# Kernel tuning notes

Measured on AMD Instinct MI355X. Metric: run time of the kernel, lower is better.

Reference implementation:

```python
import jax, jax.numpy as jnp
import numpy as np

E, I, H, T = 8, 2816, 1024, 8192

def setup_inputs() -> dict:
    key = jax.random.key(0)
    ks = jax.random.split(key, 5)
    scale_w = 1.0 / np.sqrt(H)
    return {
        "hidden_states": jax.random.normal(ks[0], (T, H), jnp.float32),
        "router_logits": jax.random.normal(ks[1], (T, E), jnp.float32),
        "W1": jax.random.normal(ks[2], (E, I, H), jnp.float32) * scale_w,
        "W3": jax.random.normal(ks[3], (E, I, H), jnp.float32) * scale_w,
        "W2": jax.random.normal(ks[4], (E, H, I), jnp.float32) * (1.0 / np.sqrt(I)),
        "top_k": 2,
    }

def reference(hidden_states, router_logits, W1, W3, W2, top_k):
    # softmax router in fp32, topk, renormalize (renormalize=True, use_grouped_topk=False)
    probs = jax.nn.softmax(router_logits.astype(jnp.float32), axis=-1)  # [T,E]
    vals, idx = jax.lax.top_k(probs, top_k)                             # [T,K]
    vals = vals / jnp.sum(vals, axis=-1, keepdims=True)
    vals = vals.astype(hidden_states.dtype)
    n_tok, n_exp = probs.shape
    # dense per-token expert weight matrix [T,E]; zero for unrouted experts,
    # mathematically identical to the gather/scatter-add in the ipex op
    w = jnp.zeros((n_tok, n_exp), hidden_states.dtype).at[
        jnp.arange(n_tok)[:, None], idx].add(vals)

    def expert_step(acc, args):
        We1, We3, We2, we = args  # [I,H], [I,H], [H,I], [T]
        h = jax.nn.silu(hidden_states @ We1.T) * (hidden_states @ We3.T)  # [T,I]
        return acc + we[:, None] * (h @ We2.T), None

    out, _ = jax.lax.scan(expert_step, jnp.zeros_like(hidden_states),
                          (W1, W3, W2, w.T))
    return out
```

## Files before the change

### kernel.cpp

```cpp
#include <hip/hip_runtime.h>
#include <stdint.h>

#define NE 8
#define NI 2816
#define NH 1024
#define NT 8192
#define NPAIR (NT * 2)

typedef __bf16 bf16x8 __attribute__((ext_vector_type(8)));
typedef float f32x4 __attribute__((ext_vector_type(4)));

__device__ __forceinline__ uint16_t f2bf(float f) {
    union { float f; uint32_t u; } v;
    v.f = f;
    return (uint16_t)((v.u + 0x7FFFu + ((v.u >> 16) & 1u)) >> 16);
}

__device__ __forceinline__ float bflo(uint32_t u) {
    union { uint32_t x; float f; } v; v.x = u << 16; return v.f;
}
__device__ __forceinline__ float bfhi(uint32_t u) {
    union { uint32_t x; float f; } v; v.x = u & 0xffff0000u; return v.f;
}

__device__ __forceinline__ void gld16(const void* g, void* l) {
    __builtin_amdgcn_global_load_lds(
        (__attribute__((address_space(1))) void*)(uintptr_t)g,
        (__attribute__((address_space(3))) void*)(uint32_t)(uintptr_t)l,
        16, 0, 0);
}

__global__ __launch_bounds__(256) void k_cvt3(const float* __restrict__ W1,
                                              const float* __restrict__ W3,
                                              const float* __restrict__ W2,
                                              uint16_t* __restrict__ W1b,
                                              uint16_t* __restrict__ W3b,
                                              uint16_t* __restrict__ W2b) {
    int i = blockIdx.x * 256 + threadIdx.x;
    const float* s = blockIdx.y == 0 ? W1 : (blockIdx.y == 1 ? W3 : W2);
    uint16_t* d = blockIdx.y == 0 ? W1b : (blockIdx.y == 1 ? W3b : W2b);
    float4 a = ((const float4*)s)[(size_t)i * 2];
    float4 b = ((const float4*)s)[(size_t)i * 2 + 1];
    uint4 o;
    o.x = (uint32_t)f2bf(a.x) | ((uint32_t)f2bf(a.y) << 16);
    o.y = (uint32_t)f2bf(a.z) | ((uint32_t)f2bf(a.w) << 16);
    o.z = (uint32_t)f2bf(b.x) | ((uint32_t)f2bf(b.y) << 16);
    o.w = (uint32_t)f2bf(b.z) | ((uint32_t)f2bf(b.w) << 16);
    ((uint4*)d)[i] = o;
}

__global__ __launch_bounds__(256) void k_router(const float* __restrict__ logits,
                                                int* __restrict__ tok_e,
                                                float2* __restrict__ tok_w,
                                                int* __restrict__ counts) {
    int t = blockIdx.x * 256 + threadIdx.x;
    if (t >= NT) return;
    float4 a = ((const float4*)logits)[(size_t)t * 2];
    float4 b = ((const float4*)logits)[(size_t)t * 2 + 1];
    float l[8] = {a.x, a.y, a.z, a.w, b.x, b.y, b.z, b.w};
    int i0 = 0; float l0 = l[0];
#pragma unroll
    for (int e = 1; e < 8; e++) if (l[e] > l0) { l0 = l[e]; i0 = e; }
    int i1 = -1; float l1 = -3.4e38f;
#pragma unroll
    for (int e = 0; e < 8; e++) if (e != i0 && l[e] > l1) { l1 = l[e]; i1 = e; }
    float w0 = 1.f / (1.f + __expf(l1 - l0));
    float w1 = 1.f - w0;
    tok_e[t] = i0 | (i1 << 8);
    tok_w[t] = make_float2(w0, w1);
    atomicAdd(&counts[i0], 1);
    atomicAdd(&counts[i1], 1);
}

__global__ void k_scan(const int* __restrict__ counts, int* __restrict__ offsets,
                       int* __restrict__ cursor) {
    if (threadIdx.x == 0) {
        int o = 0;
        for (int e = 0; e < NE; e++) { offsets[e] = o; cursor[e] = o; o += counts[e]; }
    }
}

__global__ __launch_bounds__(128) void k_gather(const float* __restrict__ x,
                                                const int* __restrict__ tok_e,
                                                const float2* __restrict__ tok_w,
                                                int* __restrict__ cursor,
                                                uint16_t* __restrict__ Xg,
                                                int2* __restrict__ tok_slots,
                                                float* __restrict__ slot_w) {
    int t = blockIdx.x;
    __shared__ int ss[2];
    if (threadIdx.x == 0) {
        int ee = tok_e[t];
        float2 w = tok_w[t];
        int s0 = atomicAdd(&cursor[ee & 0xff], 1);
        int s1 = atomicAdd(&cursor[(ee >> 8) & 0xff], 1);
        ss[0] = s0; ss[1] = s1;
        tok_slots[t] = make_int2(s0, s1);
        slot_w[s0] = w.x;
        slot_w[s1] = w.y;
    }
    __syncthreads();
    int s0 = ss[0], s1 = ss[1];
    int i = threadIdx.x;
    const float4* xr = (const float4*)(x + (size_t)t * NH);
    float4 a = xr[i * 2];
    float4 b = xr[i * 2 + 1];
    uint4 o;
    o.x = (uint32_t)f2bf(a.x) | ((uint32_t)f2bf(a.y) << 16);
    o.y = (uint32_t)f2bf(a.z) | ((uint32_t)f2bf(a.w) << 16);
    o.z = (uint32_t)f2bf(b.x) | ((uint32_t)f2bf(b.y) << 16);
    o.w = (uint32_t)f2bf(b.z) | ((uint32_t)f2bf(b.w) << 16);
    ((uint4*)(Xg + (size_t)s0 * NH))[i] = o;
    ((uint4*)(Xg + (size_t)s1 * NH))[i] = o;
}

__global__ __launch_bounds__(256, 2) void k_gemm1(const uint16_t* __restrict__ Xg,
                                                  const uint16_t* __restrict__ W1b,
                                                  const uint16_t* __restrict__ W3b,
                                                  uint16_t* __restrict__ Hbuf,
                                                  const int* __restrict__ counts,
                                                  const int* __restrict__ offsets) {
    int e = blockIdx.z;
    int n_e = counts[e];
    int mtile = blockIdx.y;
    if (mtile * 128 >= n_e) return;
    int ntile = blockIdx.x;
    int off = offsets[e];

    __shared__ __align__(16) uint16_t As[128 * 32];
    __shared__ __align__(16) uint16_t B1s[128 * 32];
    __shared__ __align__(16) uint16_t B3s[128 * 32];

    int tid = threadIdx.x;
    int r = tid >> 2, c = tid & 3;
    int wv = tid >> 6, lane = tid & 63;
    int wr = wv >> 1, wc = wv & 1;
    int m_in = lane & 15, q = lane >> 4;

    int rowA0 = off + mtile * 128 + r;
    int rowA1 = min(rowA0 + 64, NPAIR - 1);
    rowA0 = min(rowA0, NPAIR - 1);
    const uint16_t* a0 = Xg + (size_t)rowA0 * NH + c * 8;
    const uint16_t* a1 = Xg + (size_t)rowA1 * NH + c * 8;
    const uint16_t* b1r = W1b + ((size_t)e * NI + ntile * 128 + r) * NH + c * 8;
    const uint16_t* b3r = W3b + ((size_t)e * NI + ntile * 128 + r) * NH + c * 8;

    uint16_t* lA0 = &As[tid * 8];   uint16_t* lA1 = &As[2048 + tid * 8];
    uint16_t* lB10 = &B1s[tid * 8]; uint16_t* lB11 = &B1s[2048 + tid * 8];
    uint16_t* lB30 = &B3s[tid * 8]; uint16_t* lB31 = &B3s[2048 + tid * 8];

    const uint16_t* pa = &As[(wr * 64 + m_in) * 32 + q * 8];
    const uint16_t* pb1 = &B1s[(wc * 64 + m_in) * 32 + q * 8];
    const uint16_t* pb3 = &B3s[(wc * 64 + m_in) * 32 + q * 8];

    f32x4 acc1[4][4] = {};
    f32x4 acc3[4][4] = {};

    for (int k0 = 0; k0 < NH; k0 += 32) {
        gld16(a0 + k0, lA0);
        gld16(a1 + k0, lA1);
        gld16(b1r + k0, lB10);
        gld16(b1r + (size_t)64 * NH + k0, lB11);
        gld16(b3r + k0, lB30);
        gld16(b3r + (size_t)64 * NH + k0, lB31);
        __syncthreads();

        bf16x8 af[4], b1f[4], b3f[4];
#pragma unroll
        for (int it = 0; it < 4; it++) af[it] = *(const bf16x8*)(pa + it * 512);
#pragma unroll
        for (int jt = 0; jt < 4; jt++) {
            b1f[jt] = *(const bf16x8*)(pb1 + jt * 512);
            b3f[jt] = *(const bf16x8*)(pb3 + jt * 512);
        }
#pragma unroll
        for (int it = 0; it < 4; it++)
#pragma unroll
            for (int jt = 0; jt < 4; jt++) {
                acc1[it][jt] = __builtin_amdgcn_mfma_f32_16x16x32_bf16(af[it], b1f[jt], acc1[it][jt], 0, 0, 0);
                acc3[it][jt] = __builtin_amdgcn_mfma_f32_16x16x32_bf16(af[it], b3f[jt], acc3[it][jt], 0, 0, 0);
            }
        __syncthreads();
    }

    int sBase = off + mtile * 128;
#pragma unroll
    for (int it = 0; it < 4; it++) {
#pragma unroll
        for (int reg = 0; reg < 4; reg++) {
            int lm = wr * 64 + it * 16 + q * 4 + reg;
            if (mtile * 128 + lm < n_e) {
                uint16_t* orow = Hbuf + (size_t)(sBase + lm) * NI + ntile * 128 + wc * 64 + m_in;
#pragma unroll
                for (int jt = 0; jt < 4; jt++) {
                    float c1 = acc1[it][jt][reg];
                    float c3 = acc3[it][jt][reg];
                    float hv = (c1 / (1.f + __expf(-c1))) * c3;
                    orow[jt * 16] = f2bf(hv);
                }
            }
        }
    }
}

__global__ __launch_bounds__(256, 2) void k_gemm2(const uint16_t* __restrict__ Hbuf,
                                                  const uint16_t* __restrict__ W2b,
                                                  uint16_t* __restrict__ Ybuf,
                                                  const int* __restrict__ counts,
                                                  const int* __restrict__ offsets) {
    int e = blockIdx.z;
    int n_e = counts[e];
    int mtile = blockIdx.y;
    if (mtile * 128 >= n_e) return;
    int ntile = blockIdx.x;
    int off = offsets[e];

    __shared__ __align__(16) uint16_t As[128 * 32];
    __shared__ __align__(16) uint16_t Bs[128 * 32];

    int tid = threadIdx.x;
    int r = tid >> 2, c = tid & 3;
    int wv = tid >> 6, lane = tid & 63;
    int wr = wv >> 1, wc = wv & 1;
    int m_in = lane & 15, q = lane >> 4;

    int rowA0 = off + mtile * 128 + r;
    int rowA1 = min(rowA0 + 64, NPAIR - 1);
    rowA0 = min(rowA0, NPAIR - 1);
    const uint16_t* a0 = Hbuf + (size_t)rowA0 * NI + c * 8;
    const uint16_t* a1 = Hbuf + (size_t)rowA1 * NI + c * 8;
    const uint16_t* br = W2b + ((size_t)e * NH + ntile * 128 + r) * NI + c * 8;

    uint16_t* lA0 = &As[tid * 8]; uint16_t* lA1 = &As[2048 + tid * 8];
    uint16_t* lB0 = &Bs[tid * 8]; uint16_t* lB1 = &Bs[2048 + tid * 8];

    const uint16_t* pa = &As[(wr * 64 + m_in) * 32 + q * 8];
    const uint16_t* pb = &Bs[(wc * 64 + m_in) * 32 + q * 8];

    f32x4 acc[4][4] = {};

    for (int k0 = 0; k0 < NI; k0 += 32) {
        gld16(a0 + k0, lA0);
        gld16(a1 + k0, lA1);
        gld16(br + k0, lB0);
        gld16(br + (size_t)64 * NI + k0, lB1);
        __syncthreads();

        bf16x8 af[4], bf[4];
#pragma unroll
        for (int it = 0; it < 4; it++) af[it] = *(const bf16x8*)(pa + it * 512);
#pragma unroll
        for (int jt = 0; jt < 4; jt++) bf[jt] = *(const bf16x8*)(pb + jt * 512);
#pragma unroll
        for (int it = 0; it < 4; it++)
#pragma unroll
            for (int jt = 0; jt < 4; jt++)
                acc[it][jt] = __builtin_amdgcn_mfma_f32_16x16x32_bf16(af[it], bf[jt], acc[it][jt], 0, 0, 0);
        __syncthreads();
    }

    int sBase = off + mtile * 128;
#pragma unroll
    for (int it = 0; it < 4; it++) {
#pragma unroll
        for (int reg = 0; reg < 4; reg++) {
            int lm = wr * 64 + it * 16 + q * 4 + reg;
            if (mtile * 128 + lm < n_e) {
                uint16_t* orow = Ybuf + (size_t)(sBase + lm) * NH + ntile * 128 + wc * 64 + m_in;
#pragma unroll
                for (int jt = 0; jt < 4; jt++)
                    orow[jt * 16] = f2bf(acc[it][jt][reg]);
            }
        }
    }
}

__global__ __launch_bounds__(256) void k_combine(const uint16_t* __restrict__ Y,
                                                 const int2* __restrict__ tok_slots,
                                                 const float* __restrict__ slot_w,
                                                 float* __restrict__ out) {
    int idx = blockIdx.x * 256 + threadIdx.x;
    int t = idx >> 7;
    int g = idx & 127;
    int2 s = tok_slots[t];
    float w0 = slot_w[s.x], w1 = slot_w[s.y];
    uint4 u0 = ((const uint4*)(Y + (size_t)s.x * NH))[g];
    uint4 u1 = ((const uint4*)(Y + (size_t)s.y * NH))[g];
    float4 o0, o1;
    o0.x = w0 * bflo(u0.x) + w1 * bflo(u1.x);
    o0.y = w0 * bfhi(u0.x) + w1 * bfhi(u1.x);
    o0.z = w0 * bflo(u0.y) + w1 * bflo(u1.y);
    o0.w = w0 * bfhi(u0.y) + w1 * bfhi(u1.y);
    o1.x = w0 * bflo(u0.z) + w1 * bflo(u1.z);
    o1.y = w0 * bfhi(u0.z) + w1 * bfhi(u1.z);
    o1.z = w0 * bflo(u0.w) + w1 * bflo(u1.w);
    o1.w = w0 * bfhi(u0.w) + w1 * bfhi(u1.w);
    float4* orow = (float4*)(out + (size_t)t * NH + g * 8);
    orow[0] = o0;
    orow[1] = o1;
}

extern "C" void kernel_launch(void* const* d_in, const int* in_sizes, int n_in,
                              void* d_out, int out_size, void* d_ws, size_t ws_size,
                              hipStream_t stream) {
    const float* x = (const float*)d_in[0];
    const float* logits = (const float*)d_in[1];
    const float* W1 = (const float*)d_in[2];
    const float* W3 = (const float*)d_in[3];
    const float* W2 = (const float*)d_in[4];
    float* out = (float*)d_out;

    char* ws = (char*)d_ws;
    size_t o = 0;
    auto nxt = [&](size_t b) -> void* {
        void* p = ws + o;
        o += (b + 255) & ~(size_t)255;
        return p;
    };
    const size_t WELEMS = (size_t)NE * NI * NH;
    uint16_t* W1b = (uint16_t*)nxt(WELEMS * 2);
    uint16_t* W3b = (uint16_t*)nxt(WELEMS * 2);
    uint16_t* W2b = (uint16_t*)nxt(WELEMS * 2);
    uint16_t* Xg = (uint16_t*)nxt((size_t)NPAIR * NH * 2);
    uint16_t* Hbuf = (uint16_t*)nxt((size_t)NPAIR * NI * 2);
    float* slot_w = (float*)nxt((size_t)NPAIR * 4);
    int2* tok_slots = (int2*)nxt((size_t)NT * 8);
    int* tok_e = (int*)nxt((size_t)NT * 4);
    float2* tok_w = (float2*)nxt((size_t)NT * 8);
    int* meta = (int*)nxt(128);
    int* counts = meta;
    int* offsets = meta + 8;
    int* cursor = meta + 16;
    uint16_t* Ybuf = Xg;
    (void)ws_size; (void)in_sizes; (void)n_in;

    hipMemsetAsync(meta, 0, 128, stream);

    k_router<<<NT / 256, 256, 0, stream>>>(logits, tok_e, tok_w, counts);
    k_scan<<<1, 64, 0, stream>>>(counts, offsets, cursor);

    k_cvt3<<<dim3((unsigned)(WELEMS / 8 / 256), 3), 256, 0, stream>>>(W1, W3, W2, W1b, W3b, W2b);

    k_gather<<<NT, 128, 0, stream>>>(x, tok_e, tok_w, cursor, Xg, tok_slots, slot_w);

    k_gemm1<<<dim3(NI / 128, NT / 128, NE), 256, 0, stream>>>(Xg, W1b, W3b, Hbuf, counts, offsets);
    k_gemm2<<<dim3(NH / 128, NT / 128, NE), 256, 0, stream>>>(Hbuf, W2b, Ybuf, counts, offsets);
    k_combine<<<NT * NH / 8 / 256, 256, 0, stream>>>(Ybuf, tok_slots, slot_w, out);
}
```

Before: 961.0 us.

## Use 512-thread GEMM blocks with 8 waves and XOR-swizzled LDS layout

Both expert GEMM kernels move from 256 to 512 threads per block. The 128x128 tile is now split across 8 waves of 64x32 each, so each wave holds half the accumulator registers. Each thread issues one global-to-LDS load per operand instead of two. An XOR granule permutation is applied to LDS addresses to reduce bank conflicts on fragment reads. The aim is higher occupancy and latency hiding, at the cost of more A-fragment LDS reads per wave, since each wave still loads all four A fragments for half the B columns.

```diff
diff --git a/kernel.cpp b/kernel.cpp
--- a/kernel.cpp
+++ b/kernel.cpp
@@ -28,6 +28,10 @@
         (__attribute__((address_space(1))) void*)(uintptr_t)g,
         (__attribute__((address_space(3))) void*)(uint32_t)(uintptr_t)l,
         16, 0, 0);
+}
+
+__device__ __forceinline__ int granperm(int r) {
+    return (r & 3) ^ ((r >> 2) & 3);
 }
 
 __global__ __launch_bounds__(256) void k_cvt3(const float* __restrict__ W1,
@@ -114,7 +118,7 @@
     ((uint4*)(Xg + (size_t)s1 * NH))[i] = o;
 }
 
-__global__ __launch_bounds__(256, 2) void k_gemm1(const uint16_t* __restrict__ Xg,
+__global__ __launch_bounds__(512, 4) void k_gemm1(const uint16_t* __restrict__ Xg,
                                                   const uint16_t* __restrict__ W1b,
                                                   const uint16_t* __restrict__ W3b,
                                                   uint16_t* __restrict__ Hbuf,
@@ -134,49 +138,49 @@
     int tid = threadIdx.x;
     int r = tid >> 2, c = tid & 3;
     int wv = tid >> 6, lane = tid & 63;
-    int wr = wv >> 1, wc = wv & 1;
+    int wrow = wv & 1, wcol = wv >> 1;
     int m_in = lane & 15, q = lane >> 4;
 
-    int rowA0 = off + mtile * 128 + r;
-    int rowA1 = min(rowA0 + 64, NPAIR - 1);
-    rowA0 = min(rowA0, NPAIR - 1);
-    const uint16_t* a0 = Xg + (size_t)rowA0 * NH + c * 8;
-    const uint16_t* a1 = Xg + (size_t)rowA1 * NH + c * 8;
-    const uint16_t* b1r = W1b + ((size_t)e * NI + ntile * 128 + r) * NH + c * 8;
-    const uint16_t* b3r = W3b + ((size_t)e * NI + ntile * 128 + r) * NH + c * 8;
-
-    uint16_t* lA0 = &As[tid * 8];   uint16_t* lA1 = &As[2048 + tid * 8];
-    uint16_t* lB10 = &B1s[tid * 8]; uint16_t* lB11 = &B1s[2048 + tid * 8];
-    uint16_t* lB30 = &B3s[tid * 8]; uint16_t* lB31 = &B3s[2048 + tid * 8];
-
-    const uint16_t* pa = &As[(wr * 64 + m_in) * 32 + q * 8];
-    const uint16_t* pb1 = &B1s[(wc * 64 + m_in) * 32 + q * 8];
-    const uint16_t* pb3 = &B3s[(wc * 64 + m_in) * 32 + q * 8];
-
-    f32x4 acc1[4][4] = {};
-    f32x4 acc3[4][4] = {};
+    int pg = c ^ granperm(r);
+
+    int rowA = min(off + mtile * 128 + r, NPAIR - 1);
+    const uint16_t* a0 = Xg + (size_t)rowA * NH + pg * 8;
+    const uint16_t* b1r = W1b + ((size_t)e * NI + ntile * 128 + r) * NH + pg * 8;
+    const uint16_t* b3r = W3b + ((size_t)e * NI + ntile * 128 + r) * NH + pg * 8;
+
+    uint16_t* lA = &As[tid * 8];
+    uint16_t* lB1 = &B1s[tid * 8];
+    uint16_t* lB3 = &B3s[tid * 8];
+
+    int arow = wrow * 64 + m_in;
+    int aq = q ^ granperm(arow);
+    const uint16_t* pa = &As[arow * 32 + aq * 8];
+    int brow = wcol * 32 + m_in;
+    int bq = q ^ granperm(brow);
+    const uint16_t* pb1 = &B1s[brow * 32 + bq * 8];
+    const uint16_t* pb3 = &B3s[brow * 32 + bq * 8];
+
+    f32x4 acc1[4][2] = {};
+    f32x4 acc3[4][2] = {};
 
     for (int k0 = 0; k0 < NH; k0 += 32) {
-        gld16(a0 + k0, lA0);
-        gld16(a1 + k0, lA1);
-        gld16(b1r + k0, lB10);
-        gld16(b1r + (size_t)64 * NH + k0, lB11);
-        gld16(b3r + k0, lB30);
-        gld16(b3r + (size_t)64 * NH + k0, lB31);
+        gld16(a0 + k0, lA);
+        gld16(b1r + k0, lB1);
+        gld16(b3r + k0, lB3);
         __syncthreads();
 
-        bf16x8 af[4], b1f[4], b3f[4];
+        bf16x8 af[4], b1f[2], b3f[2];
 #pragma unroll
         for (int it = 0; it < 4; it++) af[it] = *(const bf16x8*)(pa + it * 512);
 #pragma unroll
-        for (int jt = 0; jt < 4; jt++) {
+        for (int jt = 0; jt < 2; jt++) {
             b1f[jt] = *(const bf16x8*)(pb1 + jt * 512);
             b3f[jt] = *(const bf16x8*)(pb3 + jt * 512);
         }
 #pragma unroll
         for (int it = 0; it < 4; it++)
 #pragma unroll
-            for (int jt = 0; jt < 4; jt++) {
+            for (int jt = 0; jt < 2; jt++) {
                 acc1[it][jt] = __builtin_amdgcn_mfma_f32_16x16x32_bf16(af[it], b1f[jt], acc1[it][jt], 0, 0, 0);
                 acc3[it][jt] = __builtin_amdgcn_mfma_f32_16x16x32_bf16(af[it], b3f[jt], acc3[it][jt], 0, 0, 0);
             }
@@ -188,11 +192,11 @@
     for (int it = 0; it < 4; it++) {
 #pragma unroll
         for (int reg = 0; reg < 4; reg++) {
-            int lm = wr * 64 + it * 16 + q * 4 + reg;
+            int lm = wrow * 64 + it * 16 + q * 4 + reg;
             if (mtile * 128 + lm < n_e) {
-                uint16_t* orow = Hbuf + (size_t)(sBase + lm) * NI + ntile * 128 + wc * 64 + m_in;
-#pragma unroll
-                for (int jt = 0; jt < 4; jt++) {
+                uint16_t* orow = Hbuf + (size_t)(sBase + lm) * NI + ntile * 128 + wcol * 32 + m_in;
+#pragma unroll
+                for (int jt = 0; jt < 2; jt++) {
                     float c1 = acc1[it][jt][reg];
                     float c3 = acc3[it][jt][reg];
                     float hv = (c1 / (1.f + __expf(-c1))) * c3;
@@ -203,7 +207,7 @@
     }
 }
 
-__global__ __launch_bounds__(256, 2) void k_gemm2(const uint16_t* __restrict__ Hbuf,
+__global__ __launch_bounds__(512, 6) void k_gemm2(const uint16_t* __restrict__ Hbuf,
                                                   const uint16_t* __restrict__ W2b,
                                                   uint16_t* __restrict__ Ybuf,
                                                   const int* __restrict__ counts,
@@ -221,40 +225,41 @@
     int tid = threadIdx.x;
     int r = tid >> 2, c = tid & 3;
     int wv = tid >> 6, lane = tid & 63;
-    int wr = wv >> 1, wc = wv & 1;
+    int wrow = wv & 1, wcol = wv >> 1;
     int m_in = lane & 15, q = lane >> 4;
 
-    int rowA0 = off + mtile * 128 + r;
-    int rowA1 = min(rowA0 + 64, NPAIR - 1);
-    rowA0 = min(rowA0, NPAIR - 1);
-    const uint16_t* a0 = Hbuf + (size_t)rowA0 * NI + c * 8;
-    const uint16_t* a1 = Hbuf + (size_t)rowA1 * NI + c * 8;
-    const uint16_t* br = W2b + ((size_t)e * NH + ntile * 128 + r) * NI + c * 8;
-
-    uint16_t* lA0 = &As[tid * 8]; uint16_t* lA1 = &As[2048 + tid * 8];
-    uint16_t* lB0 = &Bs[tid * 8]; uint16_t* lB1 = &Bs[2048 + tid * 8];
-
-    const uint16_t* pa = &As[(wr * 64 + m_in) * 32 + q * 8];
-    const uint16_t* pb = &Bs[(wc * 64 + m_in) * 32 + q * 8];
-
-    f32x4 acc[4][4] = {};
+    int pg = c ^ granperm(r);
+
+    int rowA = min(off + mtile * 128 + r, NPAIR - 1);
+    const uint16_t* a0 = Hbuf + (size_t)rowA * NI + pg * 8;
+    const uint16_t* br = W2b + ((size_t)e * NH + ntile * 128 + r) * NI + pg * 8;
+
+    uint16_t* lA = &As[tid * 8];
+    uint16_t* lB = &Bs[tid * 8];
+
+    int arow = wrow * 64 + m_in;
+    int aq = q ^ granperm(arow);
+    const uint16_t* pa = &As[arow * 32 + aq * 8];
+    int brow = wcol * 32 + m_in;
+    int bq = q ^ granperm(brow);
+    const uint16_t* pb = &Bs[brow * 32 + bq * 8];
+
+    f32x4 acc[4][2] = {};
 
     for (int k0 = 0; k0 < NI; k0 += 32) {
-        gld16(a0 + k0, lA0);
-        gld16(a1 + k0, lA1);
-        gld16(br + k0, lB0);
-        gld16(br + (size_t)64 * NI + k0, lB1);
+        gld16(a0 + k0, lA);
+        gld16(br + k0, lB);
         __syncthreads();
 
-        bf16x8 af[4], bf[4];
+        bf16x8 af[4], bf[2];
 #pragma unroll
         for (int it = 0; it < 4; it++) af[it] = *(const bf16x8*)(pa + it * 512);
 #pragma unroll
-        for (int jt = 0; jt < 4; jt++) bf[jt] = *(const bf16x8*)(pb + jt * 512);
+        for (int jt = 0; jt < 2; jt++) bf[jt] = *(const bf16x8*)(pb + jt * 512);
 #pragma unroll
         for (int it = 0; it < 4; it++)
 #pragma unroll
-            for (int jt = 0; jt < 4; jt++)
+            for (int jt = 0; jt < 2; jt++)
                 acc[it][jt] = __builtin_amdgcn_mfma_f32_16x16x32_bf16(af[it], bf[jt], acc[it][jt], 0, 0, 0);
         __syncthreads();
     }
@@ -264,11 +269,11 @@
     for (int it = 0; it < 4; it++) {
 #pragma unroll
         for (int reg = 0; reg < 4; reg++) {
-            int lm = wr * 64 + it * 16 + q * 4 + reg;
+            int lm = wrow * 64 + it * 16 + q * 4 + reg;
             if (mtile * 128 + lm < n_e) {
-                uint16_t* orow = Ybuf + (size_t)(sBase + lm) * NH + ntile * 128 + wc * 64 + m_in;
-#pragma unroll
-                for (int jt = 0; jt < 4; jt++)
+                uint16_t* orow = Ybuf + (size_t)(sBase + lm) * NH + ntile * 128 + wcol * 32 + m_in;
+#pragma unroll
+                for (int jt = 0; jt < 2; jt++)
                     orow[jt * 16] = f2bf(acc[it][jt][reg]);
             }
         }
@@ -343,7 +348,7 @@
 
     k_gather<<<NT, 128, 0, stream>>>(x, tok_e, tok_w, cursor, Xg, tok_slots, slot_w);
 
-    k_gemm1<<<dim3(NI / 128, NT / 128, NE), 256, 0, stream>>>(Xg, W1b, W3b, Hbuf, counts, offsets);
-    k_gemm2<<<dim3(NH / 128, NT / 128, NE), 256, 0, stream>>>(Hbuf, W2b, Ybuf, counts, offsets);
+    k_gemm1<<<dim3(NI / 128, NT / 128, NE), 512, 0, stream>>>(Xg, W1b, W3b, Hbuf, counts, offsets);
+    k_gemm2<<<dim3(NH / 128, NT / 128, NE), 512, 0, stream>>>(Hbuf, W2b, Ybuf, counts, offsets);
     k_combine<<<NT * NH / 8 / 256, 256, 0, stream>>>(Ybuf, tok_slots, slot_w, out);
 }
```

New measurement: 965.4 us. Within noise of the previous version (+0.4%).
